# Performance work log

Measured on AMD Instinct MI355X. Metric: run time of the kernel, lower is better.

Reference implementation:

```python
import jax, jax.numpy as jnp
import numpy as np

HEADS = 8
DIM_HEAD = 64
DIM = 512
HIDDEN = HEADS * DIM_HEAD  # 512


def setup_inputs() -> dict:
    key = jax.random.key(0)
    k1, k2, k3, k4 = jax.random.split(key, 4)
    b, m, n = 4, 8, 512
    x = jax.random.normal(k1, (b, m, n, DIM), dtype=jnp.float32)
    pos_bias = jax.random.normal(k2, (HEADS, n, 16, 16), dtype=jnp.float32)
    # torch nn.Linear(dim, 3*hidden) weight is [3*hidden, dim]; we store the
    # transposed matmul form [dim, 3*hidden] for y = x @ W.
    w_qkv = jax.random.normal(k3, (DIM, 3 * HIDDEN), dtype=jnp.float32) * (DIM ** -0.5)
    w_out = jax.random.normal(k4, (HIDDEN, DIM), dtype=jnp.float32) * (HIDDEN ** -0.5)
    return {"x": x, "pos_bias": pos_bias, "w_qkv": w_qkv, "w_out": w_out}


def reference(x, pos_bias, w_qkv, w_out):
    b, m, n, _ = x.shape
    h, d = HEADS, DIM_HEAD
    scale = d ** -0.5
    qkv = jnp.einsum('bmnc,ce->bmne', x, w_qkv)  # [b,m,n,3*hidden]
    q, k, v = jnp.split(qkv, 3, axis=-1)
    # 'b m n (h d) -> (b m) h n d'
    def to_heads(t):
        return t.reshape(b * m, n, h, d).transpose(0, 2, 1, 3)
    q, k, v = to_heads(q), to_heads(k), to_heads(v)
    q = q * scale
    sim = jnp.einsum('bhid,bhjd->bhij', q, k)  # [(b*m), h, n, n]
    # pos_bias [h, n, p, q] -> mean over last two dims -> [h, n] -> broadcast [1,h,n,1]
    pb = pos_bias.mean(axis=(-2, -1))[None, :, :, None]
    sim = sim + pb
    sim = sim - jax.lax.stop_gradient(jnp.max(sim, axis=-1, keepdims=True))
    attn = jax.nn.softmax(sim, axis=-1)
    out = jnp.einsum('bhij,bhjd->bhid', attn, v)  # [(b*m), h, n, d]
    # '(b m) h n d -> b m n (h d)'
    out = out.transpose(0, 2, 1, 3).reshape(b, m, n, h * d)
    return jnp.einsum('bmne,ec->bmnc', out, w_out)
```

## Files before the change

kernel.cpp:

```cpp
#include <hip/hip_runtime.h>
#include <stdint.h>


typedef __attribute__((ext_vector_type(8))) short bf16x8;
typedef __attribute__((ext_vector_type(4))) float f32x4;
typedef __attribute__((ext_vector_type(4))) unsigned short us4;
typedef __attribute__((ext_vector_type(4))) float float4v;

__device__ __forceinline__ unsigned short f2b(float f) {
  union { float f; uint32_t u; } x; x.f = f;
  uint32_t r = x.u + 0x7fffu + ((x.u >> 16) & 1u);
  return (unsigned short)(r >> 16);
}

__device__ __forceinline__ uint32_t cvtpk(float lo, float hi) {
  uint32_t r;
  asm("v_cvt_pk_bf16_f32 %0, %1, %2" : "=v"(r) : "v"(lo), "v"(hi));
  return r;
}

__device__ __forceinline__ f32x4 mfma16(bf16x8 a, bf16x8 b, f32x4 c) {
  return __builtin_amdgcn_mfma_f32_16x16x32_bf16(a, b, c, 0, 0, 0);
}

__device__ __forceinline__ void gload_lds16(const unsigned short* g, unsigned short* l) {
  __builtin_amdgcn_global_load_lds(
      (const __attribute__((address_space(1))) unsigned int*)g,
      (__attribute__((address_space(3))) unsigned int*)l, 16, 0, 0);
}

__global__ __launch_bounds__(256) void prep_kernel(
    const float* __restrict__ x, unsigned short* __restrict__ xb,
    const float* __restrict__ wq, unsigned short* __restrict__ wqbT,
    const float* __restrict__ wo, unsigned short* __restrict__ wobT) {
  const int bid = blockIdx.x;
  if (bid < 8192) {
    size_t i = ((size_t)bid * 256 + threadIdx.x) * 4;
    float4v v = *(const float4v*)(x + i);
    us4 o;
#pragma unroll
    for (int j = 0; j < 4; ++j) o[j] = f2b(v[j]);
    *(us4*)(xb + i) = o;
    return;
  }
  __shared__ float tile[64][65];
  const float* src;
  unsigned short* dst;
  int R, C, bx, by;
  float scl = 1.0f;
  if (bid < 8192 + 192) {
    int q = bid - 8192;
    src = wq; dst = wqbT; R = 512; C = 1536; bx = q % 24; by = q / 24;
    if (bx * 64 < 512) scl = 0.125f;
  } else {
    int q = bid - 8384;
    src = wo; dst = wobT; R = 512; C = 512; bx = q % 8; by = q / 8;
  }
  const int tc0 = bx * 64, tr0 = by * 64;
#pragma unroll
  for (int k2 = 0; k2 < 16; ++k2) {
    int idx = threadIdx.x + k2 * 256;
    int r = idx >> 6, c = idx & 63;
    tile[r][c] = src[(size_t)(tr0 + r) * C + tc0 + c];
  }
  __syncthreads();
#pragma unroll
  for (int k2 = 0; k2 < 16; ++k2) {
    int idx = threadIdx.x + k2 * 256;
    int c = idx >> 6, r = idx & 63;
    dst[(size_t)(tc0 + c) * R + tr0 + r] = f2b(tile[r][c] * scl);
  }
}

__device__ __forceinline__ void gemm_core(
    const unsigned short* __restrict__ A, const unsigned short* __restrict__ Bt,
    int r0, int c0, unsigned short* As, unsigned short* Bs,
    f32x4 (&acc)[4][4]) {
  const int tid = threadIdx.x;
  const int lane = tid & 63;
  const int wave = tid >> 6;
  const int wr = (wave >> 1) * 64;
  const int wc = (wave & 1) * 64;
  const int l15 = lane & 15;
  const int g = lane >> 4;
  const int lsw = l15 & 7;

#pragma unroll
  for (int m = 0; m < 4; ++m)
#pragma unroll
    for (int n = 0; n < 4; ++n) acc[m][n] = (f32x4){0.f, 0.f, 0.f, 0.f};

  auto stage = [&](int kt, int b) {
#pragma unroll
    for (int i = 0; i < 4; ++i) {
      int chunk = tid + i * 256;
      int row = chunk >> 3;
      int csw = (chunk & 7) ^ (row & 7);
      gload_lds16(A + (size_t)(r0 + row) * 512 + kt + csw * 8,
                  As + b * 8192 + chunk * 8);
      gload_lds16(Bt + (size_t)(c0 + row) * 512 + kt + csw * 8,
                  Bs + b * 8192 + chunk * 8);
    }
  };

  stage(0, 0);
  asm volatile("s_waitcnt vmcnt(0)" ::: "memory");
  __builtin_amdgcn_s_barrier();

  int cur = 0;
#pragma unroll
  for (int t = 0; t < 8; ++t) {
    if (t < 7) stage((t + 1) * 64, cur ^ 1);
    const unsigned short* as = As + cur * 8192;
    const unsigned short* bs = Bs + cur * 8192;
#pragma unroll
    for (int ks = 0; ks < 2; ++ks) {
      bf16x8 af[4], bfr[4];
      const int cj = ((g + ks * 4) ^ lsw) * 8;
#pragma unroll
      for (int m = 0; m < 4; ++m)
        af[m] = *(const bf16x8*)(as + (wr + m * 16 + l15) * 64 + cj);
#pragma unroll
      for (int n = 0; n < 4; ++n)
        bfr[n] = *(const bf16x8*)(bs + (wc + n * 16 + l15) * 64 + cj);
      __builtin_amdgcn_s_setprio(1);
#pragma unroll
      for (int m = 0; m < 4; ++m)
#pragma unroll
        for (int n = 0; n < 4; ++n) acc[m][n] = mfma16(af[m], bfr[n], acc[m][n]);
      __builtin_amdgcn_s_setprio(0);
    }
    if (t < 7) {
      asm volatile("s_waitcnt vmcnt(0)" ::: "memory");
      __builtin_amdgcn_s_barrier();
      cur ^= 1;
    }
  }
  __syncthreads();
}

__global__ __launch_bounds__(256) void gemm_qkv_kernel(
    const unsigned short* __restrict__ xb, const unsigned short* __restrict__ wqbT,
    unsigned short* __restrict__ qb, unsigned short* __restrict__ kb,
    unsigned short* __restrict__ vtb) {
  __shared__ unsigned short smem[32768];
  f32x4 acc[4][4];
  const int bid = blockIdx.x;
  const int wgid = (bid & 7) * 192 + (bid >> 3);
  const int r0 = (wgid / 12) * 128;
  const int c0 = (wgid % 12) * 128;
  gemm_core(xb, wqbT, r0, c0, smem, smem + 16384, acc);

  const int tid = threadIdx.x, lane = tid & 63, wave = tid >> 6;
  const int wr = (wave >> 1) * 64, wc = (wave & 1) * 64;
  const int l15 = lane & 15, g = lane >> 4;
  const int part = c0 >> 9;

  if (part < 2) {
#pragma unroll
    for (int m = 0; m < 4; ++m) {
      int rbase = wr + m * 16 + 4 * g;
#pragma unroll
      for (int n = 0; n < 4; ++n) {
        int c = wc + n * 16 + l15;
        int c2 = c >> 3, ci = c & 7;
#pragma unroll
        for (int rr = 0; rr < 4; ++rr) {
          int r = rbase + rr;
          smem[r * 128 + ((c2 ^ (r & 15)) << 3) + ci] = f2b(acc[m][n][rr]);
        }
      }
    }
    __syncthreads();
    unsigned short* dstb = (part == 0) ? qb : kb;
#pragma unroll
    for (int it = 0; it < 8; ++it) {
      int idx = tid + it * 256;
      int r = idx >> 4, c2 = idx & 15;
      bf16x8 v = *(const bf16x8*)(smem + r * 128 + ((c2 ^ (r & 15)) << 3));
      int e = c0 + c2 * 8;
      int rem = e & 511, h = rem >> 6, d = rem & 63;
      int ig = r0 + r;
      int bh = (ig >> 9) * 8 + h, i = ig & 511;
      *(bf16x8*)(dstb + ((size_t)bh * 512 + i) * 64 + d) = v;
    }
  } else {
#pragma unroll
    for (int m = 0; m < 4; ++m) {
      int rbase = wr + m * 16 + 4 * g;
      int r2 = rbase >> 3, rhalf = rbase & 7;
#pragma unroll
      for (int n = 0; n < 4; ++n) {
        int c = wc + n * 16 + l15;
        us4 v;
#pragma unroll
        for (int rr = 0; rr < 4; ++rr) v[rr] = f2b(acc[m][n][rr]);
        *(us4*)(smem + c * 128 + ((r2 ^ (c & 15)) << 3) + rhalf) = v;
      }
    }
    __syncthreads();
#pragma unroll
    for (int it = 0; it < 8; ++it) {
      int idx = tid + it * 256;
      int c = idx >> 4, r8 = idx & 15;
      bf16x8 v = *(const bf16x8*)(smem + c * 128 + ((r8 ^ (c & 15)) << 3));
      int e = c0 + c;
      int rem = e & 511, h = rem >> 6, d = rem & 63;
      int ig0 = r0 + r8 * 8;
      int bh = (ig0 >> 9) * 8 + h, i = ig0 & 511;
      *(bf16x8*)(vtb + ((size_t)bh * 64 + d) * 512 + i) = v;
    }
  }
}

__global__ __launch_bounds__(256) void gemm_out_kernel(
    const unsigned short* __restrict__ ao, const unsigned short* __restrict__ wobT,
    float* __restrict__ out) {
  __shared__ unsigned short smem[32768];
  f32x4 acc[4][4];
  const int bid = blockIdx.x;
  const int wgid = (bid & 7) * 64 + (bid >> 3);
  const int r0 = (wgid >> 2) * 128;
  const int c0 = (wgid & 3) * 128;
  gemm_core(ao, wobT, r0, c0, smem, smem + 16384, acc);

  const int tid = threadIdx.x, lane = tid & 63, wave = tid >> 6;
  const int wr = (wave >> 1) * 64, wc = (wave & 1) * 64;
  const int l15 = lane & 15, g = lane >> 4;
#pragma unroll
  for (int m = 0; m < 4; ++m) {
    int i0g = r0 + wr + m * 16 + 4 * g;
#pragma unroll
    for (int n = 0; n < 4; ++n) {
      int e = c0 + wc + n * 16 + l15;
#pragma unroll
      for (int rr = 0; rr < 4; ++rr)
        out[(size_t)(i0g + rr) * 512 + e] = acc[m][n][rr];
    }
  }
}

__global__ __launch_bounds__(512, 4) void attn_kernel(
    const unsigned short* __restrict__ qb, const unsigned short* __restrict__ kb,
    const unsigned short* __restrict__ vtb, unsigned short* __restrict__ ao) {
  __shared__ unsigned short kbuf[2][8192];
  __shared__ unsigned short vbuf[2][8192];
  __shared__ unsigned short Ps[8][16][40];
  const int bid = blockIdx.x;
  const int wgid = (bid & 7) * 128 + (bid >> 3);
  const int bh = wgid >> 2;
  const int qt = wgid & 3;
  const int tid = threadIdx.x, lane = tid & 63, wave = tid >> 6;
  const int l15 = lane & 15, g = lane >> 4;
  const int qrow0 = qt * 128 + wave * 16;

  const unsigned short* Q = qb + ((size_t)bh * 512 + qrow0) * 64;
  const unsigned short* Kp = kb + (size_t)bh * 512 * 64;
  const unsigned short* Vt = vtb + (size_t)bh * 64 * 512;

  bf16x8 qf0 = *(const bf16x8*)(Q + l15 * 64 + g * 8);
  bf16x8 qf1 = *(const bf16x8*)(Q + l15 * 64 + 32 + g * 8);

  const int krow = tid >> 3;
  const int kck = (tid & 7) ^ (krow & 7);
  const int vrow = tid >> 4;
  const int vck = (tid & 15) ^ (vrow & 15);

  auto stage = [&](int t, int b) {
    const unsigned short* ks = Kp + ((size_t)t * 128 + krow) * 64 + kck * 8;
    gload_lds16(ks, kbuf[b] + tid * 8);
    gload_lds16(ks + 64 * 64, kbuf[b] + tid * 8 + 4096);
    const unsigned short* vs = Vt + (size_t)vrow * 512 + t * 128 + vck * 8;
    gload_lds16(vs, vbuf[b] + tid * 8);
    gload_lds16(vs + 32 * 512, vbuf[b] + tid * 8 + 4096);
  };

  f32x4 oacc[4];
#pragma unroll
  for (int m = 0; m < 4; ++m) oacc[m] = (f32x4){0.f, 0.f, 0.f, 0.f};
  float srow[4] = {0.f, 0.f, 0.f, 0.f};

  stage(0, 0);
  asm volatile("s_waitcnt vmcnt(0)" ::: "memory");
  __builtin_amdgcn_s_barrier();

  int cur = 0;
#pragma unroll
  for (int t = 0; t < 4; ++t) {
    if (t < 3) stage(t + 1, cur ^ 1);

    const unsigned short* kb_ = kbuf[cur];
    f32x4 s[8];
    const int c0i = g ^ (l15 & 7);
    __builtin_amdgcn_s_setprio(1);
#pragma unroll
    for (int tt = 0; tt < 8; ++tt) {
      int row = tt * 16 + l15;
      bf16x8 b0 = *(const bf16x8*)(kb_ + (row * 8 + c0i) * 8);
      bf16x8 b1 = *(const bf16x8*)(kb_ + (row * 8 + (c0i ^ 4)) * 8);
      f32x4 c = (f32x4){0.f, 0.f, 0.f, 0.f};
      c = mfma16(qf0, b0, c);
      s[tt] = mfma16(qf1, b1, c);
    }
    __builtin_amdgcn_s_setprio(0);

#pragma unroll
    for (int tt = 0; tt < 8; ++tt)
#pragma unroll
      for (int rr = 0; rr < 4; ++rr) {
        float e = __expf(s[tt][rr]);
        s[tt][rr] = e;
        srow[rr] += e;
      }

    const unsigned short* vb_ = vbuf[cur];
#pragma unroll
    for (int cc = 0; cc < 4; ++cc) {
#pragma unroll
      for (int rr = 0; rr < 4; ++rr) {
        uint32_t pk = cvtpk(s[cc * 2][rr], s[cc * 2 + 1][rr]);
        Ps[wave][4 * g + rr][l15] = (unsigned short)pk;
        Ps[wave][4 * g + rr][16 + l15] = (unsigned short)(pk >> 16);
      }
      asm volatile("s_waitcnt lgkmcnt(0)" ::: "memory");
      bf16x8 pf = *(const bf16x8*)(&Ps[wave][l15][g * 8]);
      __builtin_amdgcn_s_setprio(1);
#pragma unroll
      for (int m = 0; m < 4; ++m) {
        int vr = m * 16 + l15;
        bf16x8 vf = *(const bf16x8*)(vb_ + (vr * 16 + ((cc * 4 + g) ^ l15)) * 8);
        oacc[m] = mfma16(vf, pf, oacc[m]);
      }
      __builtin_amdgcn_s_setprio(0);
    }

    if (t < 3) {
      asm volatile("s_waitcnt vmcnt(0)" ::: "memory");
      __builtin_amdgcn_s_barrier();
      cur ^= 1;
    }
  }

#pragma unroll
  for (int rr = 0; rr < 4; ++rr)
#pragma unroll
    for (int o = 1; o < 16; o <<= 1) srow[rr] += __shfl_xor(srow[rr], o);
  int srcl = (l15 >> 2) * 16;
  float t0 = __shfl(srow[0], srcl), t1 = __shfl(srow[1], srcl);
  float t2 = __shfl(srow[2], srcl), t3 = __shfl(srow[3], srcl);
  int rq = l15 & 3;
  float sq = rq == 0 ? t0 : rq == 1 ? t1 : rq == 2 ? t2 : t3;
  float invq = 1.0f / sq;

  const int hh = bh & 7, bm = bh >> 3;
  unsigned short* aorow = ao + ((size_t)bm * 512 + qrow0 + l15) * 512 + hh * 64;
#pragma unroll
  for (int m = 0; m < 4; ++m) {
    union { us4 u; uint32_t w[2]; } uv;
    uv.w[0] = cvtpk(oacc[m][0] * invq, oacc[m][1] * invq);
    uv.w[1] = cvtpk(oacc[m][2] * invq, oacc[m][3] * invq);
    *(us4*)(aorow + m * 16 + 4 * g) = uv.u;
  }
}

extern "C" void kernel_launch(void* const* d_in, const int* in_sizes, int n_in,
                              void* d_out, int out_size, void* d_ws, size_t ws_size,
                              hipStream_t stream) {
  const float* x = (const float*)d_in[0];
  const float* w_qkv = (const float*)d_in[2];
  const float* w_out = (const float*)d_in[3];
  float* out = (float*)d_out;

  char* ws = (char*)d_ws;
  const size_t SZ_XB = 16384ull * 512 * 2;
  const size_t SZ_WQ = 1536ull * 512 * 2;
  const size_t SZ_WO = 512ull * 512 * 2;
  const size_t SZ_HB = 256ull * 512 * 64 * 2;
  unsigned short* xb = (unsigned short*)(ws);
  unsigned short* wqbT = (unsigned short*)(ws + SZ_XB);
  unsigned short* wobT = (unsigned short*)(ws + SZ_XB + SZ_WQ);
  unsigned short* qb = (unsigned short*)(ws + SZ_XB + SZ_WQ + SZ_WO);
  unsigned short* kb = (unsigned short*)(ws + SZ_XB + SZ_WQ + SZ_WO + SZ_HB);
  unsigned short* vtb = (unsigned short*)(ws + SZ_XB + SZ_WQ + SZ_WO + 2 * SZ_HB);
  unsigned short* ao = (unsigned short*)(ws + SZ_XB + SZ_WQ + SZ_WO + 3 * SZ_HB);

  prep_kernel<<<8448, 256, 0, stream>>>(x, xb, w_qkv, wqbT, w_out, wobT);
  gemm_qkv_kernel<<<1536, 256, 0, stream>>>(xb, wqbT, qb, kb, vtb);
  attn_kernel<<<1024, 512, 0, stream>>>(qb, kb, vtb, ao);
  gemm_out_kernel<<<512, 256, 0, stream>>>(ao, wobT, out);
}
```

Baseline: 89.83 us.

## Fuse fp32-to-bf16 conversion of x into the QKV GEMM tile loads

Removes the separate pass that converted x to bf16 in a workspace buffer. The QKV GEMM now loads fp32 x tiles directly into LDS with an XOR swizzle and converts them to bf16 in registers before the MFMAs, using a K step of 32 instead of 64. This drops a full read-and-write pass over the 32 MB input, but doubles the A-side LDS and global bytes per tile and the number of K iterations. Each GEMM block now also does conversion work, and x is re-read by all 12 column tiles.

```diff
diff --git a/kernel.cpp b/kernel.cpp
--- a/kernel.cpp
+++ b/kernel.cpp
@@ -23,37 +23,26 @@
   return __builtin_amdgcn_mfma_f32_16x16x32_bf16(a, b, c, 0, 0, 0);
 }
 
-__device__ __forceinline__ void gload_lds16(const unsigned short* g, unsigned short* l) {
+__device__ __forceinline__ void gload_lds16(const void* g, void* l) {
   __builtin_amdgcn_global_load_lds(
       (const __attribute__((address_space(1))) unsigned int*)g,
       (__attribute__((address_space(3))) unsigned int*)l, 16, 0, 0);
 }
 
 __global__ __launch_bounds__(256) void prep_kernel(
-    const float* __restrict__ x, unsigned short* __restrict__ xb,
     const float* __restrict__ wq, unsigned short* __restrict__ wqbT,
     const float* __restrict__ wo, unsigned short* __restrict__ wobT) {
+  __shared__ float tile[64][65];
   const int bid = blockIdx.x;
-  if (bid < 8192) {
-    size_t i = ((size_t)bid * 256 + threadIdx.x) * 4;
-    float4v v = *(const float4v*)(x + i);
-    us4 o;
-#pragma unroll
-    for (int j = 0; j < 4; ++j) o[j] = f2b(v[j]);
-    *(us4*)(xb + i) = o;
-    return;
-  }
-  __shared__ float tile[64][65];
   const float* src;
   unsigned short* dst;
   int R, C, bx, by;
   float scl = 1.0f;
-  if (bid < 8192 + 192) {
-    int q = bid - 8192;
-    src = wq; dst = wqbT; R = 512; C = 1536; bx = q % 24; by = q / 24;
+  if (bid < 192) {
+    src = wq; dst = wqbT; R = 512; C = 1536; bx = bid % 24; by = bid / 24;
     if (bx * 64 < 512) scl = 0.125f;
   } else {
-    int q = bid - 8384;
+    int q = bid - 192;
     src = wo; dst = wobT; R = 512; C = 512; bx = q % 8; by = q / 8;
   }
   const int tc0 = bx * 64, tr0 = by * 64;
@@ -69,6 +58,149 @@
     int idx = threadIdx.x + k2 * 256;
     int c = idx >> 6, r = idx & 63;
     dst[(size_t)(tc0 + c) * R + tr0 + r] = f2b(tile[r][c] * scl);
+  }
+}
+
+__global__ __launch_bounds__(256) void gemm_qkv_kernel(
+    const float* __restrict__ x, const unsigned short* __restrict__ wqbT,
+    unsigned short* __restrict__ qb, unsigned short* __restrict__ kb,
+    unsigned short* __restrict__ vtb) {
+  __shared__ unsigned short smem[24576];
+  unsigned short* As = smem;
+  unsigned short* Bs = smem + 16384;
+  const int tid = threadIdx.x;
+  const int lane = tid & 63, wave = tid >> 6;
+  const int wr = (wave >> 1) * 64, wc = (wave & 1) * 64;
+  const int l15 = lane & 15, g = lane >> 4;
+  const int rsw = (l15 >> 1) & 3;
+  const int bid = blockIdx.x;
+  const int wgid = (bid & 7) * 192 + (bid >> 3);
+  const int r0 = (wgid / 12) * 128;
+  const int c0 = (wgid % 12) * 128;
+
+  f32x4 acc[4][4];
+#pragma unroll
+  for (int m = 0; m < 4; ++m)
+#pragma unroll
+    for (int n = 0; n < 4; ++n) acc[m][n] = (f32x4){0.f, 0.f, 0.f, 0.f};
+
+  auto stage = [&](int t, int b) {
+#pragma unroll
+    for (int i = 0; i < 4; ++i) {
+      int chunk = tid + i * 256;
+      int row = chunk >> 3;
+      int csw = (chunk & 7) ^ (row & 7);
+      gload_lds16(x + (size_t)(r0 + row) * 512 + t * 32 + csw * 4,
+                  As + b * 8192 + chunk * 8);
+    }
+#pragma unroll
+    for (int i = 0; i < 2; ++i) {
+      int chunk = tid + i * 256;
+      int row = chunk >> 2;
+      int csw = (chunk & 3) ^ ((row >> 1) & 3);
+      gload_lds16(wqbT + (size_t)(c0 + row) * 512 + t * 32 + csw * 8,
+                  Bs + b * 4096 + chunk * 8);
+    }
+  };
+
+  stage(0, 0);
+  asm volatile("s_waitcnt vmcnt(0)" ::: "memory");
+  __builtin_amdgcn_s_barrier();
+
+  int cur = 0;
+#pragma unroll
+  for (int t = 0; t < 16; ++t) {
+    if (t < 15) stage(t + 1, cur ^ 1);
+    const f32x4* a32 = (const f32x4*)(As + cur * 8192);
+    const unsigned short* bs = Bs + cur * 4096;
+    bf16x8 af[4], bfr[4];
+    const int s0 = (2 * g) ^ (l15 & 7);
+    const int s1 = (2 * g + 1) ^ (l15 & 7);
+#pragma unroll
+    for (int m = 0; m < 4; ++m) {
+      int rl = wr + m * 16 + l15;
+      f32x4 lo = a32[rl * 8 + s0];
+      f32x4 hi = a32[rl * 8 + s1];
+      union { bf16x8 v; uint32_t w[4]; } u;
+      u.w[0] = cvtpk(lo[0], lo[1]);
+      u.w[1] = cvtpk(lo[2], lo[3]);
+      u.w[2] = cvtpk(hi[0], hi[1]);
+      u.w[3] = cvtpk(hi[2], hi[3]);
+      af[m] = u.v;
+    }
+#pragma unroll
+    for (int n = 0; n < 4; ++n)
+      bfr[n] = *(const bf16x8*)(bs + ((wc + n * 16 + l15) * 4 + (g ^ rsw)) * 8);
+    __builtin_amdgcn_s_setprio(1);
+#pragma unroll
+    for (int m = 0; m < 4; ++m)
+#pragma unroll
+      for (int n = 0; n < 4; ++n) acc[m][n] = mfma16(af[m], bfr[n], acc[m][n]);
+    __builtin_amdgcn_s_setprio(0);
+    if (t < 15) {
+      asm volatile("s_waitcnt vmcnt(0)" ::: "memory");
+      __builtin_amdgcn_s_barrier();
+      cur ^= 1;
+    }
+  }
+  __syncthreads();
+
+  const int part = c0 >> 9;
+
+  if (part < 2) {
+#pragma unroll
+    for (int m = 0; m < 4; ++m) {
+      int rbase = wr + m * 16 + 4 * g;
+#pragma unroll
+      for (int n = 0; n < 4; ++n) {
+        int c = wc + n * 16 + l15;
+        int c2 = c >> 3, ci = c & 7;
+#pragma unroll
+        for (int rr = 0; rr < 4; ++rr) {
+          int r = rbase + rr;
+          smem[r * 128 + ((c2 ^ (r & 15)) << 3) + ci] = f2b(acc[m][n][rr]);
+        }
+      }
+    }
+    __syncthreads();
+    unsigned short* dstb = (part == 0) ? qb : kb;
+#pragma unroll
+    for (int it = 0; it < 8; ++it) {
+      int idx = tid + it * 256;
+      int r = idx >> 4, c2 = idx & 15;
+      bf16x8 v = *(const bf16x8*)(smem + r * 128 + ((c2 ^ (r & 15)) << 3));
+      int e = c0 + c2 * 8;
+      int rem = e & 511, h = rem >> 6, d = rem & 63;
+      int ig = r0 + r;
+      int bh = (ig >> 9) * 8 + h, i = ig & 511;
+      *(bf16x8*)(dstb + ((size_t)bh * 512 + i) * 64 + d) = v;
+    }
+  } else {
+#pragma unroll
+    for (int m = 0; m < 4; ++m) {
+      int rbase = wr + m * 16 + 4 * g;
+      int r2 = rbase >> 3, rhalf = rbase & 7;
+#pragma unroll
+      for (int n = 0; n < 4; ++n) {
+        int c = wc + n * 16 + l15;
+        us4 v;
+#pragma unroll
+        for (int rr = 0; rr < 4; ++rr) v[rr] = f2b(acc[m][n][rr]);
+        *(us4*)(smem + c * 128 + ((r2 ^ (c & 15)) << 3) + rhalf) = v;
+      }
+    }
+    __syncthreads();
+#pragma unroll
+    for (int it = 0; it < 8; ++it) {
+      int idx = tid + it * 256;
+      int c = idx >> 4, r8 = idx & 15;
+      bf16x8 v = *(const bf16x8*)(smem + c * 128 + ((r8 ^ (c & 15)) << 3));
+      int e = c0 + c;
+      int rem = e & 511, h = rem >> 6, d = rem & 63;
+      int ig0 = r0 + r8 * 8;
+      int bh = (ig0 >> 9) * 8 + h, i = ig0 & 511;
+      *(bf16x8*)(vtb + ((size_t)bh * 64 + d) * 512 + i) = v;
+    }
   }
 }
 
@@ -137,80 +269,6 @@
     }
   }
   __syncthreads();
-}
-
-__global__ __launch_bounds__(256) void gemm_qkv_kernel(
-    const unsigned short* __restrict__ xb, const unsigned short* __restrict__ wqbT,
-    unsigned short* __restrict__ qb, unsigned short* __restrict__ kb,
-    unsigned short* __restrict__ vtb) {
-  __shared__ unsigned short smem[32768];
-  f32x4 acc[4][4];
-  const int bid = blockIdx.x;
-  const int wgid = (bid & 7) * 192 + (bid >> 3);
-  const int r0 = (wgid / 12) * 128;
-  const int c0 = (wgid % 12) * 128;
-  gemm_core(xb, wqbT, r0, c0, smem, smem + 16384, acc);
-
-  const int tid = threadIdx.x, lane = tid & 63, wave = tid >> 6;
-  const int wr = (wave >> 1) * 64, wc = (wave & 1) * 64;
-  const int l15 = lane & 15, g = lane >> 4;
-  const int part = c0 >> 9;
-
-  if (part < 2) {
-#pragma unroll
-    for (int m = 0; m < 4; ++m) {
-      int rbase = wr + m * 16 + 4 * g;
-#pragma unroll
-      for (int n = 0; n < 4; ++n) {
-        int c = wc + n * 16 + l15;
-        int c2 = c >> 3, ci = c & 7;
-#pragma unroll
-        for (int rr = 0; rr < 4; ++rr) {
-          int r = rbase + rr;
-          smem[r * 128 + ((c2 ^ (r & 15)) << 3) + ci] = f2b(acc[m][n][rr]);
-        }
-      }
-    }
-    __syncthreads();
-    unsigned short* dstb = (part == 0) ? qb : kb;
-#pragma unroll
-    for (int it = 0; it < 8; ++it) {
-      int idx = tid + it * 256;
-      int r = idx >> 4, c2 = idx & 15;
-      bf16x8 v = *(const bf16x8*)(smem + r * 128 + ((c2 ^ (r & 15)) << 3));
-      int e = c0 + c2 * 8;
-      int rem = e & 511, h = rem >> 6, d = rem & 63;
-      int ig = r0 + r;
-      int bh = (ig >> 9) * 8 + h, i = ig & 511;
-      *(bf16x8*)(dstb + ((size_t)bh * 512 + i) * 64 + d) = v;
-    }
-  } else {
-#pragma unroll
-    for (int m = 0; m < 4; ++m) {
-      int rbase = wr + m * 16 + 4 * g;
-      int r2 = rbase >> 3, rhalf = rbase & 7;
-#pragma unroll
-      for (int n = 0; n < 4; ++n) {
-        int c = wc + n * 16 + l15;
-        us4 v;
-#pragma unroll
-        for (int rr = 0; rr < 4; ++rr) v[rr] = f2b(acc[m][n][rr]);
-        *(us4*)(smem + c * 128 + ((r2 ^ (c & 15)) << 3) + rhalf) = v;
-      }
-    }
-    __syncthreads();
-#pragma unroll
-    for (int it = 0; it < 8; ++it) {
-      int idx = tid + it * 256;
-      int c = idx >> 4, r8 = idx & 15;
-      bf16x8 v = *(const bf16x8*)(smem + c * 128 + ((r8 ^ (c & 15)) << 3));
-      int e = c0 + c;
-      int rem = e & 511, h = rem >> 6, d = rem & 63;
-      int ig0 = r0 + r8 * 8;
-      int bh = (ig0 >> 9) * 8 + h, i = ig0 & 511;
-      *(bf16x8*)(vtb + ((size_t)bh * 64 + d) * 512 + i) = v;
-    }
-  }
 }
 
 __global__ __launch_bounds__(256) void gemm_out_kernel(
@@ -372,20 +430,18 @@
   float* out = (float*)d_out;
 
   char* ws = (char*)d_ws;
-  const size_t SZ_XB = 16384ull * 512 * 2;
   const size_t SZ_WQ = 1536ull * 512 * 2;
   const size_t SZ_WO = 512ull * 512 * 2;
   const size_t SZ_HB = 256ull * 512 * 64 * 2;
-  unsigned short* xb = (unsigned short*)(ws);
-  unsigned short* wqbT = (unsigned short*)(ws + SZ_XB);
-  unsigned short* wobT = (unsigned short*)(ws + SZ_XB + SZ_WQ);
-  unsigned short* qb = (unsigned short*)(ws + SZ_XB + SZ_WQ + SZ_WO);
-  unsigned short* kb = (unsigned short*)(ws + SZ_XB + SZ_WQ + SZ_WO + SZ_HB);
-  unsigned short* vtb = (unsigned short*)(ws + SZ_XB + SZ_WQ + SZ_WO + 2 * SZ_HB);
-  unsigned short* ao = (unsigned short*)(ws + SZ_XB + SZ_WQ + SZ_WO + 3 * SZ_HB);
-
-  prep_kernel<<<8448, 256, 0, stream>>>(x, xb, w_qkv, wqbT, w_out, wobT);
-  gemm_qkv_kernel<<<1536, 256, 0, stream>>>(xb, wqbT, qb, kb, vtb);
+  unsigned short* wqbT = (unsigned short*)(ws);
+  unsigned short* wobT = (unsigned short*)(ws + SZ_WQ);
+  unsigned short* qb = (unsigned short*)(ws + SZ_WQ + SZ_WO);
+  unsigned short* kb = (unsigned short*)(ws + SZ_WQ + SZ_WO + SZ_HB);
+  unsigned short* vtb = (unsigned short*)(ws + SZ_WQ + SZ_WO + 2 * SZ_HB);
+  unsigned short* ao = (unsigned short*)(ws + SZ_WQ + SZ_WO + 3 * SZ_HB);
+
+  prep_kernel<<<256, 256, 0, stream>>>(w_qkv, wqbT, w_out, wobT);
+  gemm_qkv_kernel<<<1536, 256, 0, stream>>>(x, wqbT, qb, kb, vtb);
   attn_kernel<<<1024, 512, 0, stream>>>(qb, kb, vtb, ao);
   gemm_out_kernel<<<512, 256, 0, stream>>>(ao, wobT, out);
 }
```

New measurement: 92.81 us. +3.3%, slower.
